# Kernel optimization log

Measured on AMD Instinct MI355X. Metric: run time of the kernel, lower is better.

## Reference

```python
import jax, jax.numpy as jnp
import numpy as np

B, C, H, W = 32, 64, 64, 64
OC = 2 * C  # same_c=False -> out_channels = 2*in_channels


def _conv(x, w, b, stride):
    y = jax.lax.conv_general_dilated(
        x, w, (stride, stride), ((1, 1), (1, 1)),
        dimension_numbers=('NCHW', 'OIHW', 'NCHW'))
    return y + b[None, :, None, None]


def _lrelu(x):
    return jnp.where(x >= 0, x, 0.1 * x)


def _roi_align_full(x, ph, pw, sr=2):
    # torchvision RoIAlign, aligned=False, spatial_scale=1, sampling_ratio=2,
    # single ROI per batch item covering [0, 0, W-1, H-1].
    b, c, h, w = x.shape
    bin_h = max(float(h - 1), 1.0) / ph
    bin_w = max(float(w - 1), 1.0) / pw
    off = (jnp.arange(sr, dtype=jnp.float32) + 0.5) / sr
    ys = ((jnp.arange(ph, dtype=jnp.float32)[:, None] + off[None, :]).reshape(-1) * bin_h)  # [ph*sr]
    xs = ((jnp.arange(pw, dtype=jnp.float32)[:, None] + off[None, :]).reshape(-1) * bin_w)  # [pw*sr]
    y0 = jnp.floor(ys).astype(jnp.int32)
    x0 = jnp.floor(xs).astype(jnp.int32)
    y1 = jnp.minimum(y0 + 1, h - 1)
    x1 = jnp.minimum(x0 + 1, w - 1)
    ly = ys - y0.astype(jnp.float32); hy = 1.0 - ly
    lx = xs - x0.astype(jnp.float32); hx = 1.0 - lx
    # gather 4 bilinear corners: [B, C, ph*sr, pw*sr]
    v00 = x[:, :, y0][:, :, :, x0]
    v01 = x[:, :, y0][:, :, :, x1]
    v10 = x[:, :, y1][:, :, :, x0]
    v11 = x[:, :, y1][:, :, :, x1]
    val = (hy[:, None] * hx[None, :]) * v00 + (hy[:, None] * lx[None, :]) * v01 \
        + (ly[:, None] * hx[None, :]) * v10 + (ly[:, None] * lx[None, :]) * v11
    # average the sr x sr samples per bin
    return val.reshape(b, c, ph, sr, pw, sr).mean(axis=(3, 5))


def setup_inputs() -> dict:
    key = jax.random.key(0)
    ks = jax.random.split(key, 20)
    def p(k, shape):
        return jax.random.normal(k, shape, dtype=jnp.float32) * 0.05
    return {
        'out1': jax.random.normal(ks[0], (B, C, H, W), dtype=jnp.float32),
        'out2': jax.random.normal(ks[1], (B, C, H, W), dtype=jnp.float32),
        'out3': jax.random.normal(ks[2], (B, C, H, W), dtype=jnp.float32),
        'w1': p(ks[3], (OC, C, 3, 3)),      'b1': p(ks[4], (OC,)),
        'w2': p(ks[5], (OC, OC, 3, 3)),     'b2': p(ks[6], (OC,)),
        'w3': p(ks[7], (OC, OC, 3, 3)),     'b3': p(ks[8], (OC,)),
        'w_aux': p(ks[9], (OC, OC, 3, 3)),  'b_aux': p(ks[10], (OC,)),
        'w_b2': p(ks[11], (OC, 2 * OC, 3, 3)), 'b_b2': p(ks[12], (OC,)),
        'w_prev': p(ks[13], (OC, 2 * C, 3, 3)), 'b_prev': p(ks[14], (OC,)),
        'lin_w': p(ks[15], (H * W, C)),     'lin_b': p(ks[16], (H * W,)),
    }


def reference(out1, out2, out3, w1, b1, w2, b2, w3, b3,
              w_aux, b_aux, w_b2, b_b2, w_prev, b_prev, lin_w, lin_b):
    bsz, c, h, w = out1.shape
    l1 = _lrelu(_conv(out1, w1, b1, 1))
    l2 = _lrelu(_conv(l1, w2, b2, 1))
    l3 = _lrelu(_conv(l2, w3, b3, 1))
    roi1 = _roi_align_full(l2, h // 2, w // 2)
    aux = _lrelu(_conv(l3, w_aux, b_aux, 2))        # dropout = identity (eval)
    block_out1 = roi1 + aux
    block_out2 = _lrelu(_conv(jnp.concatenate([l1, l2], axis=1), w_b2, b_b2, 2))
    prev = _lrelu(_conv(jnp.concatenate([out2, out3], axis=1), w_prev, b_prev, 1))
    # fused per-pixel attention: logits[b,p] = <lin_w[p], out1[b,:,p]> + lin_b[p]
    xp = out1.reshape(bsz, c, h * w)                 # [B, C, P], P row-major over (h, w)
    logits = jnp.einsum('bcp,pc->bp', xp, lin_w) + lin_b
    attn = jax.nn.softmax(logits, axis=-1).reshape(bsz, 1, h, w)
    block_out3 = _roi_align_full(prev * attn, h // 2, w // 2)
    return jnp.stack([block_out1 + block_out2 + block_out3, block_out2, block_out3])
```

## Files before the change

kernel.cpp:

```cpp
#include <hip/hip_runtime.h>
#include <hip/hip_bf16.h>

typedef __attribute__((ext_vector_type(8))) short short8;
typedef __attribute__((ext_vector_type(4))) float f32x4;

constexpr int B = 32, C = 64, HW = 4096;

__device__ __forceinline__ unsigned short f2bf(float f) {
    __hip_bfloat16 h = __float2bfloat16(f);
    unsigned short u; __builtin_memcpy(&u, &h, 2); return u;
}
__device__ __forceinline__ float b2f(unsigned short u) {
    unsigned int t = ((unsigned int)u) << 16; float f; __builtin_memcpy(&f, &t, 4); return f;
}
__device__ __forceinline__ void gllds16(const void* g, void* l) {
    __builtin_amdgcn_global_load_lds((const __attribute__((address_space(1))) unsigned int*)g,
                                     (__attribute__((address_space(3))) unsigned int*)l, 16, 0, 0);
}

__global__ __launch_bounds__(256) void tr_k(const float* __restrict__ out1,
                                            const float* __restrict__ out2,
                                            const float* __restrict__ out3,
                                            unsigned short* __restrict__ t1,
                                            unsigned short* __restrict__ tp)
{
    int t = threadIdx.x;
    int px = blockIdx.x * 256 + t;
    int b = blockIdx.y;
    if (blockIdx.z == 0) {
        const float* src = out1 + (size_t)b * 64 * HW + px;
        unsigned short v[64];
#pragma unroll
        for (int c = 0; c < 64; ++c) v[c] = f2bf(src[(size_t)c * HW]);
        unsigned short* dst = t1 + ((size_t)b * HW + px) * 64;
#pragma unroll
        for (int j = 0; j < 8; ++j)
            *(short8*)(dst + j * 8) = *(short8*)(v + j * 8);
    } else {
        const float* s2 = out2 + (size_t)b * 64 * HW + px;
        const float* s3 = out3 + (size_t)b * 64 * HW + px;
        unsigned short v[128];
#pragma unroll
        for (int c = 0; c < 64; ++c) v[c] = f2bf(s2[(size_t)c * HW]);
#pragma unroll
        for (int c = 0; c < 64; ++c) v[64 + c] = f2bf(s3[(size_t)c * HW]);
        unsigned short* dst = tp + ((size_t)b * HW + px) * 128;
#pragma unroll
        for (int j = 0; j < 16; ++j)
            *(short8*)(dst + j * 8) = *(short8*)(v + j * 8);
    }
}

__global__ __launch_bounds__(256) void logits_k(const float* __restrict__ out1,
                                                const float* __restrict__ lin_w,
                                                const float* __restrict__ lin_b,
                                                float* __restrict__ logits)
{
    int b = blockIdx.x >> 4;
    int p = (blockIdx.x & 15) * 256 + threadIdx.x;
    float acc = lin_b[p];
    const float* xb = out1 + (size_t)b * C * HW + p;
    const float* wp = lin_w + (size_t)p * C;
#pragma unroll
    for (int c = 0; c < C; c += 4) {
        float4 w4 = *(const float4*)(wp + c);
        acc = fmaf(xb[(size_t)c * HW],       w4.x, acc);
        acc = fmaf(xb[(size_t)(c + 1) * HW], w4.y, acc);
        acc = fmaf(xb[(size_t)(c + 2) * HW], w4.z, acc);
        acc = fmaf(xb[(size_t)(c + 3) * HW], w4.w, acc);
    }
    logits[(size_t)b * HW + p] = acc;
}

__global__ __launch_bounds__(256) void softmax_k(const float* __restrict__ logits,
                                                 float* __restrict__ attn)
{
    int b = blockIdx.x, tid = threadIdx.x;
    float lg[16];
#pragma unroll
    for (int k = 0; k < 16; ++k) lg[k] = logits[(size_t)b * HW + tid + (k << 8)];
    __shared__ float red[256];
    float m = -INFINITY;
#pragma unroll
    for (int k = 0; k < 16; ++k) m = fmaxf(m, lg[k]);
    red[tid] = m; __syncthreads();
    for (int s = 128; s > 0; s >>= 1) {
        if (tid < s) red[tid] = fmaxf(red[tid], red[tid + s]);
        __syncthreads();
    }
    m = red[0]; __syncthreads();
    float se = 0.f;
#pragma unroll
    for (int k = 0; k < 16; ++k) { lg[k] = __expf(lg[k] - m); se += lg[k]; }
    red[tid] = se; __syncthreads();
    for (int s = 128; s > 0; s >>= 1) {
        if (tid < s) red[tid] += red[tid + s];
        __syncthreads();
    }
    float inv = 1.0f / red[0];
#pragma unroll
    for (int k = 0; k < 16; ++k)
        attn[(size_t)b * HW + tid + (k << 8)] = lg[k] * inv;
}

__global__ __launch_bounds__(256) void wprep_k(const float* w1, const float* w2, const float* w3,
                                               const float* wa, const float* wb2, const float* wp,
                                               unsigned short* __restrict__ wT)
{
    int blk = blockIdx.x;
    int base, ic, l2ic, off; const float* src;
    if      (blk < 32)  { base = 0;   ic = 64;  l2ic = 6; off = 0;      src = w1;  }
    else if (blk < 96)  { base = 32;  ic = 128; l2ic = 7; off = 73728;  src = w2;  }
    else if (blk < 160) { base = 96;  ic = 128; l2ic = 7; off = 221184; src = w3;  }
    else if (blk < 224) { base = 160; ic = 128; l2ic = 7; off = 368640; src = wa;  }
    else if (blk < 352) { base = 224; ic = 256; l2ic = 8; off = 516096; src = wb2; }
    else                { base = 352; ic = 128; l2ic = 7; off = 811008; src = wp;  }
    int pair = (blk - base) * 256 + threadIdx.x;
    int oc = pair >> l2ic, icx = pair & (ic - 1);
    const float* s = src + ((size_t)(oc * ic + icx)) * 9;
#pragma unroll
    for (int k = 0; k < 9; ++k)
        wT[(size_t)off + ((size_t)(k * 128 + oc)) * ic + icx] = f2bf(s[k]);
}

template<int IC, int STRIDE, int PS_IN, int CO_IN, int OPS, int OCO, bool ATTN>
__global__ __launch_bounds__(256, 4) void conv_k(
    const unsigned short* __restrict__ in,
    const unsigned short* __restrict__ wTc,
    const float* __restrict__ bias,
    const float* __restrict__ attn,
    unsigned short* __restrict__ out)
{
    constexpr int NICG = IC / 32;
    constexpr int L = (IC == 64) ? 1 : (IC == 128) ? 2 : 3;
    constexpr int NS = 9 * NICG;
    constexpr int NPX = (STRIDE == 1) ? 4096 : 1024;
    constexpr int WO = (STRIDE == 1) ? 64 : 32;

    __shared__ char bsm[2][8192];

    int t = threadIdx.x;
    int wave = t >> 6, lane = t & 63;
    int mw = wave & 1, nw = wave >> 1;
    int l15 = lane & 15, lc = lane >> 4;
    int y0 = blockIdx.x, b = blockIdx.y;

    int bofs[4];
#pragma unroll
    for (int nf = 0; nf < 4; ++nf) {
        int oc = nw * 64 + nf * 16 + l15;
        bofs[nf] = oc * 64 + ((lc ^ ((oc >> 1) & 3)) << 4);
    }
    int oc0 = t >> 2;
    int c0 = (t & 3) ^ ((oc0 >> 1) & 3);
    const unsigned short* wsrc = wTc + oc0 * IC + c0 * 8;
    char* lbase = &bsm[0][0] + (wave << 10);

    const unsigned short* base_b = in + (size_t)b * HW * PS_IN + CO_IN + (lc << 3);
    int col[2];
#pragma unroll
    for (int f = 0; f < 2; ++f)
        col[f] = (STRIDE == 1) ? (mw * 32 + f * 16 + l15) : (f * 16 + l15);

    f32x4 acc[2][4];
#pragma unroll
    for (int f = 0; f < 2; ++f)
#pragma unroll
        for (int nf = 0; nf < 4; ++nf) acc[f][nf] = (f32x4)0.0f;

    auto stage = [&](int s, int buf) {
        int kk = s >> L, icg = s & (NICG - 1);
        const unsigned short* p = wsrc + (size_t)kk * 128 * IC + icg * 32;
        char* d = lbase + buf * 8192;
        gllds16(p, d);
        gllds16(p + 64 * IC, d + 4096);
    };

    stage(0, 0);
    __syncthreads();

    for (int s = 0; s < NS; ++s) {
        int cur = s & 1;
        if (s + 1 < NS) stage(s + 1, cur ^ 1);
        int kk = s >> L, icg = s & (NICG - 1);
        int ky = (kk * 11) >> 5;
        int kx = kk - ky * 3;
        int iy = (STRIDE == 1) ? (y0 + ky - 1) : ((y0 * 2 + mw) * 2 + ky - 1);
        bool yok = (unsigned)iy < 64u;
        const unsigned short* prow = base_b + (long)iy * (64 * PS_IN) + icg * 32;
        short8 az = {0, 0, 0, 0, 0, 0, 0, 0};
        short8 aa[2];
#pragma unroll
        for (int f = 0; f < 2; ++f) {
            int ix = (STRIDE == 1) ? (col[f] + kx - 1) : (2 * col[f] + kx - 1);
            bool ok = yok && ((unsigned)ix < 64u);
            const short8* ap = (const short8*)(prow + (long)ix * PS_IN);
            aa[f] = ok ? *ap : az;
        }
        const char* bb_base = &bsm[0][0] + cur * 8192;
        short8 bb[4];
#pragma unroll
        for (int nf = 0; nf < 4; ++nf)
            bb[nf] = *(const short8*)(bb_base + bofs[nf]);
#pragma unroll
        for (int f = 0; f < 2; ++f)
#pragma unroll
            for (int nf = 0; nf < 4; ++nf)
                acc[f][nf] = __builtin_amdgcn_mfma_f32_16x16x32_bf16(aa[f], bb[nf], acc[f][nf], 0, 0, 0);
        __syncthreads();
    }

    int orow = (STRIDE == 1) ? y0 : (y0 * 2 + mw);
    float bs[4];
#pragma unroll
    for (int nf = 0; nf < 4; ++nf) bs[nf] = bias[nw * 64 + nf * 16 + l15];
#pragma unroll
    for (int f = 0; f < 2; ++f) {
#pragma unroll
        for (int r = 0; r < 4; ++r) {
            int pxcol = ((STRIDE == 1) ? mw * 32 : 0) + f * 16 + (lc << 2) + r;
            float av = 1.0f;
            if constexpr (ATTN) av = attn[(size_t)b * HW + y0 * 64 + pxcol];
            size_t obase = ((size_t)b * NPX + (size_t)orow * WO + pxcol) * OPS + OCO;
#pragma unroll
            for (int nf = 0; nf < 4; ++nf) {
                int oc = nw * 64 + nf * 16 + l15;
                float v = acc[f][nf][r] + bs[nf];
                v = (v >= 0.0f) ? v : 0.1f * v;
                if constexpr (ATTN) v *= av;
                out[obase + oc] = f2bf(v);
            }
        }
    }
}

__device__ __forceinline__ void acc8(float* a, const unsigned short* p, float w) {
    short8 v = *(const short8*)p;
#pragma unroll
    for (int k = 0; k < 8; ++k) a[k] = fmaf(w, b2f((unsigned short)v[k]), a[k]);
}

__global__ __launch_bounds__(256) void fuse_roi_k(const unsigned short* __restrict__ prevs,
                                                  const unsigned short* __restrict__ l12,
                                                  const unsigned short* __restrict__ auxb,
                                                  const unsigned short* __restrict__ bo2b,
                                                  float* __restrict__ o0,
                                                  float* __restrict__ o1,
                                                  float* __restrict__ o2)
{
    int idx = blockIdx.x * 256 + threadIdx.x;
    int j = idx & 31, i = (idx >> 5) & 31, ocg = (idx >> 10) & 15, b = idx >> 14;
    float a3[8] = {0,0,0,0,0,0,0,0}, aR[8] = {0,0,0,0,0,0,0,0};
    const unsigned short* pb = prevs + (size_t)b * HW * 128 + ocg * 8;
    const unsigned short* lb = l12 + (size_t)b * HW * 256 + 128 + ocg * 8;
#pragma unroll
    for (int sy = 0; sy < 2; ++sy) {
        float ys = (i + 0.25f + 0.5f * sy) * 1.96875f;
        int y0 = (int)ys;
        int y1 = min(y0 + 1, 63);
        float ly = ys - (float)y0, hy = 1.0f - ly;
#pragma unroll
        for (int sx = 0; sx < 2; ++sx) {
            float xs = (j + 0.25f + 0.5f * sx) * 1.96875f;
            int x0 = (int)xs;
            int x1 = min(x0 + 1, 63);
            float lx = xs - (float)x0, hx = 1.0f - lx;
            int p00 = y0 * 64 + x0, p01 = y0 * 64 + x1, p10 = y1 * 64 + x0, p11 = y1 * 64 + x1;
            float w00 = hy * hx, w01 = hy * lx, w10 = ly * hx, w11 = ly * lx;
            acc8(a3, pb + (size_t)p00 * 128, w00); acc8(a3, pb + (size_t)p01 * 128, w01);
            acc8(a3, pb + (size_t)p10 * 128, w10); acc8(a3, pb + (size_t)p11 * 128, w11);
            acc8(aR, lb + (size_t)p00 * 256, w00); acc8(aR, lb + (size_t)p01 * 256, w01);
            acc8(aR, lb + (size_t)p10 * 256, w10); acc8(aR, lb + (size_t)p11 * 256, w11);
        }
    }
    int p32 = i * 32 + j;
    const unsigned short* ax = auxb + ((size_t)(b * 1024 + p32)) * 128 + ocg * 8;
    const unsigned short* b2 = bo2b + ((size_t)(b * 1024 + p32)) * 128 + ocg * 8;
#pragma unroll
    for (int k = 0; k < 8; ++k) {
        int oc = ocg * 8 + k;
        size_t ob = ((size_t)(b * 128 + oc)) * 1024 + p32;
        float v3 = a3[k] * 0.25f;
        float v2 = b2f(b2[k]);
        o2[ob] = v3;
        o1[ob] = v2;
        o0[ob] = aR[k] * 0.25f + b2f(ax[k]) + v2 + v3;
    }
}

extern "C" void kernel_launch(void* const* d_in, const int* in_sizes, int n_in,
                              void* d_out, int out_size, void* d_ws, size_t ws_size,
                              hipStream_t stream)
{
    const float* out1  = (const float*)d_in[0];
    const float* out2  = (const float*)d_in[1];
    const float* out3  = (const float*)d_in[2];
    const float* w1    = (const float*)d_in[3];  const float* b1    = (const float*)d_in[4];
    const float* w2    = (const float*)d_in[5];  const float* b2    = (const float*)d_in[6];
    const float* w3    = (const float*)d_in[7];  const float* b3    = (const float*)d_in[8];
    const float* w_aux = (const float*)d_in[9];  const float* b_aux = (const float*)d_in[10];
    const float* w_b2  = (const float*)d_in[11]; const float* b_b2  = (const float*)d_in[12];
    const float* w_prev= (const float*)d_in[13]; const float* b_prev= (const float*)d_in[14];
    const float* lin_w = (const float*)d_in[15]; const float* lin_b = (const float*)d_in[16];

    char* ws = (char*)d_ws;
    unsigned short* l12cat = (unsigned short*)(ws);
    unsigned short* l3     = (unsigned short*)(ws + 67108864);
    unsigned short* prevs  = l3;
    unsigned short* auxb   = (unsigned short*)(ws + 100663296);
    unsigned short* bo2b   = (unsigned short*)(ws + 109051904);
    float* attn   = (float*)(ws + 117440512);
    float* logits = (float*)(ws + 117964800);
    unsigned short* wT = (unsigned short*)(ws + 118489088);

    unsigned short* t1 = (unsigned short*)d_out;
    unsigned short* tp = t1 + (size_t)B * HW * 64;

    float* o0 = (float*)d_out;
    float* o1 = o0 + (size_t)B * 128 * 1024;
    float* o2 = o1 + (size_t)B * 128 * 1024;

    wprep_k<<<dim3(416), dim3(256), 0, stream>>>(w1, w2, w3, w_aux, w_b2, w_prev, wT);
    tr_k<<<dim3(16, B, 2), dim3(256), 0, stream>>>(out1, out2, out3, t1, tp);
    logits_k<<<dim3(B * 16), dim3(256), 0, stream>>>(out1, lin_w, lin_b, logits);
    softmax_k<<<dim3(B), dim3(256), 0, stream>>>(logits, attn);

    conv_k<64, 1, 64, 0, 256, 0, false><<<dim3(64, B), dim3(256), 0, stream>>>(
        t1, wT + 0, b1, nullptr, l12cat);
    conv_k<128, 1, 256, 0, 256, 128, false><<<dim3(64, B), dim3(256), 0, stream>>>(
        l12cat, wT + 73728, b2, nullptr, l12cat);
    conv_k<128, 1, 256, 128, 128, 0, false><<<dim3(64, B), dim3(256), 0, stream>>>(
        l12cat, wT + 221184, b3, nullptr, l3);
    conv_k<128, 2, 128, 0, 128, 0, false><<<dim3(16, B), dim3(256), 0, stream>>>(
        l3, wT + 368640, b_aux, nullptr, auxb);
    conv_k<256, 2, 256, 0, 128, 0, false><<<dim3(16, B), dim3(256), 0, stream>>>(
        l12cat, wT + 516096, b_b2, nullptr, bo2b);
    conv_k<128, 1, 128, 0, 128, 0, true><<<dim3(64, B), dim3(256), 0, stream>>>(
        tp, wT + 811008, b_prev, attn, prevs);

    fuse_roi_k<<<dim3(2048), dim3(256), 0, stream>>>(prevs, l12cat, auxb, bo2b, o0, o1, o2);
}
```

Baseline: 686.0 us.

## Use 32x32x16 MFMA conv without LDS staging and fuse logits into transpose

```diff
diff --git a/kernel.cpp b/kernel.cpp
--- a/kernel.cpp
+++ b/kernel.cpp
@@ -3,6 +3,7 @@
 
 typedef __attribute__((ext_vector_type(8))) short short8;
 typedef __attribute__((ext_vector_type(4))) float f32x4;
+typedef __attribute__((ext_vector_type(16))) float f32x16;
 
 constexpr int B = 32, C = 64, HW = 4096;
 
@@ -13,29 +14,40 @@
 __device__ __forceinline__ float b2f(unsigned short u) {
     unsigned int t = ((unsigned int)u) << 16; float f; __builtin_memcpy(&f, &t, 4); return f;
 }
-__device__ __forceinline__ void gllds16(const void* g, void* l) {
-    __builtin_amdgcn_global_load_lds((const __attribute__((address_space(1))) unsigned int*)g,
-                                     (__attribute__((address_space(3))) unsigned int*)l, 16, 0, 0);
-}
 
 __global__ __launch_bounds__(256) void tr_k(const float* __restrict__ out1,
                                             const float* __restrict__ out2,
                                             const float* __restrict__ out3,
+                                            const float* __restrict__ lin_w,
+                                            const float* __restrict__ lin_b,
                                             unsigned short* __restrict__ t1,
-                                            unsigned short* __restrict__ tp)
+                                            unsigned short* __restrict__ tp,
+                                            float* __restrict__ logits)
 {
     int t = threadIdx.x;
     int px = blockIdx.x * 256 + t;
     int b = blockIdx.y;
     if (blockIdx.z == 0) {
         const float* src = out1 + (size_t)b * 64 * HW + px;
+        const float* lwp = lin_w + (size_t)px * 64;
+        float acc = lin_b[px];
         unsigned short v[64];
 #pragma unroll
-        for (int c = 0; c < 64; ++c) v[c] = f2bf(src[(size_t)c * HW]);
+        for (int c = 0; c < 64; c += 4) {
+            float4 w4 = *(const float4*)(lwp + c);
+            float x0 = src[(size_t)c * HW];
+            float x1 = src[(size_t)(c + 1) * HW];
+            float x2 = src[(size_t)(c + 2) * HW];
+            float x3 = src[(size_t)(c + 3) * HW];
+            acc = fmaf(x0, w4.x, acc); acc = fmaf(x1, w4.y, acc);
+            acc = fmaf(x2, w4.z, acc); acc = fmaf(x3, w4.w, acc);
+            v[c] = f2bf(x0); v[c + 1] = f2bf(x1); v[c + 2] = f2bf(x2); v[c + 3] = f2bf(x3);
+        }
         unsigned short* dst = t1 + ((size_t)b * HW + px) * 64;
 #pragma unroll
         for (int j = 0; j < 8; ++j)
             *(short8*)(dst + j * 8) = *(short8*)(v + j * 8);
+        logits[(size_t)b * HW + px] = acc;
     } else {
         const float* s2 = out2 + (size_t)b * 64 * HW + px;
         const float* s3 = out3 + (size_t)b * 64 * HW + px;
@@ -49,27 +61,6 @@
         for (int j = 0; j < 16; ++j)
             *(short8*)(dst + j * 8) = *(short8*)(v + j * 8);
     }
-}
-
-__global__ __launch_bounds__(256) void logits_k(const float* __restrict__ out1,
-                                                const float* __restrict__ lin_w,
-                                                const float* __restrict__ lin_b,
-                                                float* __restrict__ logits)
-{
-    int b = blockIdx.x >> 4;
-    int p = (blockIdx.x & 15) * 256 + threadIdx.x;
-    float acc = lin_b[p];
-    const float* xb = out1 + (size_t)b * C * HW + p;
-    const float* wp = lin_w + (size_t)p * C;
-#pragma unroll
-    for (int c = 0; c < C; c += 4) {
-        float4 w4 = *(const float4*)(wp + c);
-        acc = fmaf(xb[(size_t)c * HW],       w4.x, acc);
-        acc = fmaf(xb[(size_t)(c + 1) * HW], w4.y, acc);
-        acc = fmaf(xb[(size_t)(c + 2) * HW], w4.z, acc);
-        acc = fmaf(xb[(size_t)(c + 3) * HW], w4.w, acc);
-    }
-    logits[(size_t)b * HW + p] = acc;
 }
 
 __global__ __launch_bounds__(256) void softmax_k(const float* __restrict__ logits,
@@ -131,105 +122,75 @@
     const float* __restrict__ attn,
     unsigned short* __restrict__ out)
 {
-    constexpr int NICG = IC / 32;
-    constexpr int L = (IC == 64) ? 1 : (IC == 128) ? 2 : 3;
-    constexpr int NS = 9 * NICG;
+    constexpr int NIC16 = IC / 16;
+    constexpr int LG = (IC == 64) ? 2 : (IC == 128) ? 3 : 4;
+    constexpr int NS = 9 * NIC16;
     constexpr int NPX = (STRIDE == 1) ? 4096 : 1024;
     constexpr int WO = (STRIDE == 1) ? 64 : 32;
 
-    __shared__ char bsm[2][8192];
-
     int t = threadIdx.x;
     int wave = t >> 6, lane = t & 63;
-    int mw = wave & 1, nw = wave >> 1;
-    int l15 = lane & 15, lc = lane >> 4;
+    int l31 = lane & 31, lc2 = lane >> 5;
     int y0 = blockIdx.x, b = blockIdx.y;
-
-    int bofs[4];
-#pragma unroll
-    for (int nf = 0; nf < 4; ++nf) {
-        int oc = nw * 64 + nf * 16 + l15;
-        bofs[nf] = oc * 64 + ((lc ^ ((oc >> 1) & 3)) << 4);
-    }
-    int oc0 = t >> 2;
-    int c0 = (t & 3) ^ ((oc0 >> 1) & 3);
-    const unsigned short* wsrc = wTc + oc0 * IC + c0 * 8;
-    char* lbase = &bsm[0][0] + (wave << 10);
-
-    const unsigned short* base_b = in + (size_t)b * HW * PS_IN + CO_IN + (lc << 3);
-    int col[2];
-#pragma unroll
-    for (int f = 0; f < 2; ++f)
-        col[f] = (STRIDE == 1) ? (mw * 32 + f * 16 + l15) : (f * 16 + l15);
-
-    f32x4 acc[2][4];
-#pragma unroll
-    for (int f = 0; f < 2; ++f)
-#pragma unroll
-        for (int nf = 0; nf < 4; ++nf) acc[f][nf] = (f32x4)0.0f;
-
-    auto stage = [&](int s, int buf) {
-        int kk = s >> L, icg = s & (NICG - 1);
-        const unsigned short* p = wsrc + (size_t)kk * 128 * IC + icg * 32;
-        char* d = lbase + buf * 8192;
-        gllds16(p, d);
-        gllds16(p + 64 * IC, d + 4096);
+    int col = l31;
+
+    const unsigned short* abase = in + (size_t)b * HW * PS_IN + CO_IN + lc2 * 8;
+    const unsigned short* bbase = wTc + (size_t)(wave * 32 + l31) * IC + lc2 * 8;
+    const short8 zero8 = {0, 0, 0, 0, 0, 0, 0, 0};
+
+    auto loadA = [&](int s, short8& d0, short8& d1) {
+        int kk = s >> LG, ic16 = s & (NIC16 - 1);
+        int ky = (kk * 11) >> 5, kx = kk - ky * 3;
+        int cofs = ic16 * 16;
+#pragma unroll
+        for (int m = 0; m < 2; ++m) {
+            int iy = (STRIDE == 1) ? (y0 + ky - 1) : (y0 * 4 + m * 2 + ky - 1);
+            int ix = (STRIDE == 1) ? (m * 32 + col + kx - 1) : (col * 2 + kx - 1);
+            bool ok = ((unsigned)iy < 64u) && ((unsigned)ix < 64u);
+            const unsigned short* p = abase + (long)(iy * 64 + ix) * PS_IN + cofs;
+            short8 v = ok ? *(const short8*)p : zero8;
+            if (m == 0) d0 = v; else d1 = v;
+        }
     };
-
-    stage(0, 0);
-    __syncthreads();
-
-    for (int s = 0; s < NS; ++s) {
-        int cur = s & 1;
-        if (s + 1 < NS) stage(s + 1, cur ^ 1);
-        int kk = s >> L, icg = s & (NICG - 1);
-        int ky = (kk * 11) >> 5;
-        int kx = kk - ky * 3;
-        int iy = (STRIDE == 1) ? (y0 + ky - 1) : ((y0 * 2 + mw) * 2 + ky - 1);
-        bool yok = (unsigned)iy < 64u;
-        const unsigned short* prow = base_b + (long)iy * (64 * PS_IN) + icg * 32;
-        short8 az = {0, 0, 0, 0, 0, 0, 0, 0};
-        short8 aa[2];
-#pragma unroll
-        for (int f = 0; f < 2; ++f) {
-            int ix = (STRIDE == 1) ? (col[f] + kx - 1) : (2 * col[f] + kx - 1);
-            bool ok = yok && ((unsigned)ix < 64u);
-            const short8* ap = (const short8*)(prow + (long)ix * PS_IN);
-            aa[f] = ok ? *ap : az;
-        }
-        const char* bb_base = &bsm[0][0] + cur * 8192;
-        short8 bb[4];
-#pragma unroll
-        for (int nf = 0; nf < 4; ++nf)
-            bb[nf] = *(const short8*)(bb_base + bofs[nf]);
-#pragma unroll
-        for (int f = 0; f < 2; ++f)
-#pragma unroll
-            for (int nf = 0; nf < 4; ++nf)
-                acc[f][nf] = __builtin_amdgcn_mfma_f32_16x16x32_bf16(aa[f], bb[nf], acc[f][nf], 0, 0, 0);
-        __syncthreads();
-    }
-
-    int orow = (STRIDE == 1) ? y0 : (y0 * 2 + mw);
-    float bs[4];
-#pragma unroll
-    for (int nf = 0; nf < 4; ++nf) bs[nf] = bias[nw * 64 + nf * 16 + l15];
-#pragma unroll
-    for (int f = 0; f < 2; ++f) {
-#pragma unroll
-        for (int r = 0; r < 4; ++r) {
-            int pxcol = ((STRIDE == 1) ? mw * 32 : 0) + f * 16 + (lc << 2) + r;
-            float av = 1.0f;
-            if constexpr (ATTN) av = attn[(size_t)b * HW + y0 * 64 + pxcol];
-            size_t obase = ((size_t)b * NPX + (size_t)orow * WO + pxcol) * OPS + OCO;
-#pragma unroll
-            for (int nf = 0; nf < 4; ++nf) {
-                int oc = nw * 64 + nf * 16 + l15;
-                float v = acc[f][nf][r] + bs[nf];
-                v = (v >= 0.0f) ? v : 0.1f * v;
-                if constexpr (ATTN) v *= av;
-                out[obase + oc] = f2bf(v);
-            }
+    auto loadB = [&](int s) -> short8 {
+        int kk = s >> LG, ic16 = s & (NIC16 - 1);
+        return *(const short8*)(bbase + (size_t)kk * (128 * IC) + ic16 * 16);
+    };
+
+    f32x16 acc0 = (f32x16)0.0f, acc1 = (f32x16)0.0f;
+
+    short8 A00, A01, A10, A11, B0, B1;
+    loadA(0, A00, A01);
+    B0 = loadB(0);
+
+    for (int s = 0; s < NS; s += 2) {
+        loadA(s + 1, A10, A11);
+        B1 = loadB(s + 1);
+        acc0 = __builtin_amdgcn_mfma_f32_32x32x16_bf16(A00, B0, acc0, 0, 0, 0);
+        acc1 = __builtin_amdgcn_mfma_f32_32x32x16_bf16(A01, B0, acc1, 0, 0, 0);
+        if (s + 2 < NS) {
+            loadA(s + 2, A00, A01);
+            B0 = loadB(s + 2);
+        }
+        acc0 = __builtin_amdgcn_mfma_f32_32x32x16_bf16(A10, B1, acc0, 0, 0, 0);
+        acc1 = __builtin_amdgcn_mfma_f32_32x32x16_bf16(A11, B1, acc1, 0, 0, 0);
+    }
+
+    int ocw = wave * 32 + l31;
+    float bs = bias[ocw];
+#pragma unroll
+    for (int m = 0; m < 2; ++m) {
+        f32x16 a = m ? acc1 : acc0;
+#pragma unroll
+        for (int r = 0; r < 16; ++r) {
+            int pit = (r & 3) + 8 * (r >> 2) + 4 * lc2;
+            int px = m * 32 + pit;
+            int orow = (STRIDE == 1) ? y0 : (y0 * 2 + m);
+            int ocol = (STRIDE == 1) ? px : pit;
+            float v = a[r] + bs;
+            v = (v >= 0.0f) ? v : 0.1f * v;
+            if constexpr (ATTN) v *= attn[(size_t)b * HW + y0 * 64 + px];
+            out[((size_t)b * NPX + (size_t)orow * WO + ocol) * OPS + OCO + ocw] = f2bf(v);
         }
     }
 }
@@ -321,8 +282,7 @@
     float* o2 = o1 + (size_t)B * 128 * 1024;
 
     wprep_k<<<dim3(416), dim3(256), 0, stream>>>(w1, w2, w3, w_aux, w_b2, w_prev, wT);
-    tr_k<<<dim3(16, B, 2), dim3(256), 0, stream>>>(out1, out2, out3, t1, tp);
-    logits_k<<<dim3(B * 16), dim3(256), 0, stream>>>(out1, lin_w, lin_b, logits);
+    tr_k<<<dim3(16, B, 2), dim3(256), 0, stream>>>(out1, out2, out3, lin_w, lin_b, t1, tp, logits);
     softmax_k<<<dim3(B), dim3(256), 0, stream>>>(logits, attn);
 
     conv_k<64, 1, 64, 0, 256, 0, false><<<dim3(64, B), dim3(256), 0, stream>>>(
```

Result: slower. 1.190 ms (+73.4%).
